# Optimization experiments

Measured on AMD Instinct MI355X. Metric: run time of the kernel, lower is better.

## Reference

```python
import jax, jax.numpy as jnp
import numpy as np

L, NK = 4, 6  # num blocks, Nk geodesic components

def _gelu(x):
    return jax.nn.gelu(x, approximate=False)  # torch nn.GELU default (erf)

def _ln(x, g, b, eps=1e-5):
    m = jnp.mean(x, axis=-1, keepdims=True)
    v = jnp.mean((x - m) ** 2, axis=-1, keepdims=True)
    return (x - m) * jax.lax.rsqrt(v + eps) * g + b


def setup_inputs() -> dict:
    B, N, C, M = 4, 8192, 64, 64
    key = jax.random.key(0)
    ks = iter(jax.random.split(key, 48))
    def nrm(*s):
        return jax.random.normal(next(ks), s, dtype=jnp.float32) * 0.02
    inp = {
        'x': jax.random.normal(next(ks), (B, N, 1), dtype=jnp.float32),
        'MATRIX_Phy': jax.random.normal(next(ks), (N, M), dtype=jnp.float32) * 0.02,
        'INVERSE_Phy': jax.random.normal(next(ks), (M, N), dtype=jnp.float32) * 0.02,
        'meshPoints': jax.random.normal(next(ks), (N, 3), dtype=jnp.float32),
        'adj_norm': jax.random.uniform(next(ks), (N, N), dtype=jnp.float32) / N,
    }
    inp.update(
        fc0_w=nrm(4, C), fc0_b=jnp.zeros(C), fc01_w=nrm(C, C), fc01_b=jnp.zeros(C),
        blk_ln1_g=jnp.ones((L, C)), blk_ln1_b=jnp.zeros((L, C)),
        norm1_g=jnp.ones((L, C)), norm1_b=jnp.zeros((L, C)),
        spec_w=jax.random.uniform(next(ks), (L, NK, C, C, M), dtype=jnp.float32) / (C * C),
        enc_p1_w=nrm(L, 3, C), enc_p1_b=jnp.zeros((L, C)),
        enc_p2_w=nrm(L, C, C), enc_p2_b=jnp.zeros((L, C)),
        enc_g1_w=nrm(L, C, C), enc_g1_b=jnp.zeros((L, C)),
        enc_g2_w=nrm(L, C, C), enc_g2_b=jnp.zeros((L, C)),
        enc_o1_w=nrm(L, C, 2 * C), enc_o1_b=jnp.zeros((L, 2 * C)),
        enc_o2_w=nrm(L, 2 * C, NK), enc_o2_b=jnp.zeros((L, NK)),
        spat_g1_w=nrm(L, C, 2 * C), spat_g1_b=jnp.zeros((L, 2 * C)),
        spat_g2_w=nrm(L, 2 * C, C), spat_g2_b=jnp.zeros((L, C)),
        blk_ln2_g=jnp.ones((L, C)), blk_ln2_b=jnp.zeros((L, C)),
        mlp_pre_w=nrm(L, C, 2 * C), mlp_pre_b=jnp.zeros((L, 2 * C)),
        mlp_post_w=nrm(L, 2 * C, C), mlp_post_b=jnp.zeros((L, C)),
        ln1_g=jnp.ones(C), ln1_b=jnp.zeros(C),
        fc1_w=nrm(C, 128), fc1_b=jnp.zeros(128),
        fc2_w=nrm(128, 1), fc2_b=jnp.zeros(1),
    )
    return inp


def reference(x, MATRIX_Phy, INVERSE_Phy, meshPoints, adj_norm,
              fc0_w, fc0_b, fc01_w, fc01_b,
              blk_ln1_g, blk_ln1_b, norm1_g, norm1_b, spec_w,
              enc_p1_w, enc_p1_b, enc_p2_w, enc_p2_b,
              enc_g1_w, enc_g1_b, enc_g2_w, enc_g2_b,
              enc_o1_w, enc_o1_b, enc_o2_w, enc_o2_b,
              spat_g1_w, spat_g1_b, spat_g2_w, spat_g2_b,
              blk_ln2_g, blk_ln2_b, mlp_pre_w, mlp_pre_b, mlp_post_w, mlp_post_b,
              ln1_g, ln1_b, fc1_w, fc1_b, fc2_w, fc2_b):
    B = x.shape[0]
    mesh = jnp.broadcast_to(meshPoints[None], (B,) + meshPoints.shape)  # [B,N,3]
    h = jnp.concatenate([x, mesh], axis=-1)                             # [B,N,4]
    h = h @ fc0_w + fc0_b
    h = h @ fc01_w + fc01_b                                             # [B,N,C]
    for l in range(L):
        z = _ln(h, blk_ln1_g[l], blk_ln1_b[l])
        # --- MeshGCN encoder -> geodesic mixing coefficients geoT [M,Nk] ---
        e = _gelu(meshPoints @ enc_p1_w[l] + enc_p1_b[l]) @ enc_p2_w[l] + enc_p2_b[l]
        e = _gelu(adj_norm @ (e @ enc_g1_w[l] + enc_g1_b[l]))
        e = adj_norm @ (e @ enc_g2_w[l] + enc_g2_b[l])
        e = (e @ enc_o1_w[l] + enc_o1_b[l]) @ enc_o2_w[l] + enc_o2_b[l]  # [N,Nk]
        geoT = jax.nn.softmax(INVERSE_Phy @ e, axis=1)                   # [M,Nk]
        # --- geodesic-modulated spectral conv ---
        cm = jnp.einsum('mn,bnc->bcm', INVERSE_Phy, z)                   # [B,C,M]
        w = jnp.einsum('kiom,mk->iom', spec_w[l], geoT)                  # [C,C,M]
        cg = jnp.einsum('bim,iom->bom', cm, w)                           # [B,C,M]
        x1 = jnp.einsum('bom,nm->bno', cg, MATRIX_Phy)                   # [B,N,C]
        x1 = _ln(x1, norm1_g[l], norm1_b[l])
        # --- spatial GCN branch (SimpleGCN: gcn->relu->gcn) ---
        s = jax.nn.relu(jnp.einsum('mn,bnc->bmc', adj_norm, z @ spat_g1_w[l] + spat_g1_b[l]))
        x2 = jnp.einsum('mn,bnc->bmc', adj_norm, s @ spat_g2_w[l] + spat_g2_b[l])
        h = x1 + x2 + h
        z2 = _ln(h, blk_ln2_g[l], blk_ln2_b[l])
        h = _gelu(z2 @ mlp_pre_w[l] + mlp_pre_b[l]) @ mlp_post_w[l] + mlp_post_b[l] + h
    h = _gelu(_ln(h, ln1_g, ln1_b) @ fc1_w + fc1_b)
    return h @ fc2_w + fc2_b                                             # [B,N,1]
```

## Files before the change

kernel.cpp:

```cpp
#include <hip/hip_runtime.h>
#include <math.h>

typedef __bf16 bf16_t;
typedef __bf16 bf16x8 __attribute__((ext_vector_type(8)));
typedef __bf16 bf16x4 __attribute__((ext_vector_type(4)));
typedef float  f32x4  __attribute__((ext_vector_type(4)));
typedef float  f32x16 __attribute__((ext_vector_type(16)));

#define NN 8192
#define RA 8320
#define GPS256 2129920u
#define GPS512 4259840u
#define XPAD 68
#define X2PAD 132
#define ZTPAD 66

__device__ __forceinline__ float gelu_f(float x) {
    return 0.5f * x * (1.0f + erff(x * 0.70710678118654752f));
}

__device__ __forceinline__ float wsum64(float v) {
#pragma unroll
    for (int m = 32; m; m >>= 1) v += __shfl_xor(v, m);
    return v;
}

__device__ __forceinline__ float gp4(const float* __restrict__ Gp, size_t gi) {
    return (Gp[gi] + Gp[gi + (size_t)GPS256]) + (Gp[gi + 2 * (size_t)GPS256] + Gp[gi + 3 * (size_t)GPS256]);
}

__device__ __forceinline__ float gpn(const float* __restrict__ Gp, size_t gi, size_t st, int ns) {
    float v = Gp[gi];
    for (int s = 1; s < ns; ++s) v += Gp[gi + (size_t)s * st];
    return v;
}

__device__ __forceinline__ void async16(const void* g, void* l) {
    __builtin_amdgcn_global_load_lds(
        (const __attribute__((address_space(1))) unsigned int*)g,
        (__attribute__((address_space(3))) unsigned int*)l,
        16, 0, 0);
}

__device__ __forceinline__ void mm16(const float* __restrict__ X, int xpad,
                                     const float* __restrict__ W, int ws, int K,
                                     int c, int r0, float* acc) {
    for (int k0 = 0; k0 < K; k0 += 4) {
        float w0 = W[(size_t)(k0 + 0) * ws + c];
        float w1 = W[(size_t)(k0 + 1) * ws + c];
        float w2 = W[(size_t)(k0 + 2) * ws + c];
        float w3 = W[(size_t)(k0 + 3) * ws + c];
#pragma unroll
        for (int i = 0; i < 16; ++i) {
            float4 xv = *(const float4*)(X + (size_t)(r0 + i) * xpad + k0);
            acc[i] = fmaf(xv.x, w0, acc[i]);
            acc[i] = fmaf(xv.y, w1, acc[i]);
            acc[i] = fmaf(xv.z, w2, acc[i]);
            acc[i] = fmaf(xv.w, w3, acc[i]);
        }
    }
}

__global__ __launch_bounds__(256) void k_adj_convert(const float* __restrict__ adj,
                                                     const float* __restrict__ INV,
                                                     bf16_t* __restrict__ adjB,
                                                     float* __restrict__ rowsum) {
    int row = blockIdx.x;
    int t = threadIdx.x;
    bf16_t* br = adjB + (size_t)row * NN;
    if (row >= NN + 64) {
        bf16x4 zz; zz[0] = zz[1] = zz[2] = zz[3] = (bf16_t)0.f;
#pragma unroll
        for (int v = 0; v < 8; ++v) *(bf16x4*)(br + (v * 256 + t) * 4) = zz;
        return;
    }
    const float* ar = (row < NN) ? adj + (size_t)row * NN : INV + (size_t)(row - NN) * NN;
    float s = 0.f;
#pragma unroll
    for (int v = 0; v < 8; ++v) {
        int i = (v * 256 + t) * 4;
        float4 f = *(const float4*)(ar + i);
        s += f.x + f.y + f.z + f.w;
        bf16x4 o;
        o[0] = (bf16_t)f.x; o[1] = (bf16_t)f.y; o[2] = (bf16_t)f.z; o[3] = (bf16_t)f.w;
        *(bf16x4*)(br + i) = o;
    }
    if (row < NN) {
        s = wsum64(s);
        __shared__ float w4[4];
        if ((t & 63) == 0) w4[t >> 6] = s;
        __syncthreads();
        if (t == 0) rowsum[row] = w4[0] + w4[1] + w4[2] + w4[3];
    }
}

__global__ __launch_bounds__(64) void k_fold(const float* __restrict__ fc0w, const float* __restrict__ fc0b,
                                             const float* __restrict__ fc01w, const float* __restrict__ fc01b,
                                             float* __restrict__ W0b) {
    int c = threadIdx.x;
#pragma unroll
    for (int j = 0; j < 4; ++j) {
        float a = 0.f;
        for (int k = 0; k < 64; ++k) a += fc0w[j * 64 + k] * fc01w[k * 64 + c];
        W0b[j * 64 + c] = a;
    }
    float b = fc01b[c];
    for (int k = 0; k < 64; ++k) b += fc0b[k] * fc01w[k * 64 + c];
    W0b[256 + c] = b;
}

__global__ __launch_bounds__(256) void k_init_h(const float* __restrict__ x, const float* __restrict__ mesh,
                         const float* __restrict__ W0b,
                         const float* __restrict__ zg, const float* __restrict__ zb,
                         float* __restrict__ h, bf16_t* __restrict__ Vt) {
    __shared__ __align__(16) char buf[64 * ZTPAD * 2];
    bf16_t* ZT = (bf16_t*)buf;
    int t = threadIdx.x, c = t & 63, rq = t >> 6, r0 = rq * 16;
    int bb = blockIdx.x >> 7, n0 = (blockIdx.x & 127) * 64;
    float w0c = W0b[c], w1c = W0b[64 + c], w2c = W0b[128 + c], w3c = W0b[192 + c], b0c = W0b[256 + c];
    float gc = zg[c], bc = zb[c];
#pragma unroll
    for (int q = 0; q < 16; ++q) {
        int n = n0 + r0 + q;
        int w = bb * NN + n;
        float xv = x[w];
        float m0 = mesh[n * 3], m1 = mesh[n * 3 + 1], m2 = mesh[n * 3 + 2];
        float hv = b0c + xv * w0c + m0 * w1c + m1 * w2c + m2 * w3c;
        h[(size_t)w * 64 + c] = hv;
        float s = wsum64(hv), s2 = wsum64(hv * hv);
        float mean = s * (1.f / 64.f), var = s2 * (1.f / 64.f) - mean * mean;
        float z = (hv - mean) * rsqrtf(var + 1e-5f) * gc + bc;
        ZT[c * ZTPAD + r0 + q] = (bf16_t)z;
    }
    __syncthreads();
#pragma unroll
    for (int cc = 0; cc < 16; ++cc) {
        int c2 = r0 + cc;
        Vt[(size_t)(256 + bb * 64 + c2) * NN + n0 + c] = ZT[c2 * ZTPAD + c];
    }
}

__global__ __launch_bounds__(256) void k_enc_pre(const float* __restrict__ mesh,
                          const float* __restrict__ p1w, const float* __restrict__ p1b,
                          const float* __restrict__ p2w, const float* __restrict__ p2b,
                          const float* __restrict__ g1w, const float* __restrict__ g1b,
                          bf16_t* __restrict__ Vt) {
    __shared__ __align__(16) char buf[2 * 64 * XPAD * 4];
    float* X1 = (float*)buf;
    float* X2 = (float*)(buf + 64 * XPAD * 4);
    bf16_t* ZT = (bf16_t*)buf;
    int t = threadIdx.x, c = t & 63, rq = t >> 6, r0 = rq * 16;
    int ll = blockIdx.x >> 7, n0 = (blockIdx.x & 127) * 64;
    float p1b_c = p1b[ll * 64 + c];
    float p1w0 = p1w[(ll * 3 + 0) * 64 + c], p1w1 = p1w[(ll * 3 + 1) * 64 + c], p1w2 = p1w[(ll * 3 + 2) * 64 + c];
#pragma unroll
    for (int q = 0; q < 16; ++q) {
        int n = n0 + r0 + q;
        float m0 = mesh[n * 3], m1 = mesh[n * 3 + 1], m2 = mesh[n * 3 + 2];
        X1[(r0 + q) * XPAD + c] = gelu_f(p1b_c + m0 * p1w0 + m1 * p1w1 + m2 * p1w2);
    }
    __syncthreads();
    float e2[16];
#pragma unroll
    for (int i = 0; i < 16; ++i) e2[i] = p2b[ll * 64 + c];
    mm16(X1, XPAD, p2w + ll * 4096, 64, 64, c, r0, e2);
    __syncthreads();
#pragma unroll
    for (int q = 0; q < 16; ++q) X2[(r0 + q) * XPAD + c] = e2[q];
    __syncthreads();
    float tt[16];
#pragma unroll
    for (int i = 0; i < 16; ++i) tt[i] = g1b[ll * 64 + c];
    mm16(X2, XPAD, g1w + ll * 4096, 64, 64, c, r0, tt);
#pragma unroll
    for (int q = 0; q < 16; ++q) ZT[c * ZTPAD + r0 + q] = (bf16_t)tt[q];
    __syncthreads();
#pragma unroll
    for (int cc = 0; cc < 16; ++cc) {
        int c2 = r0 + cc;
        Vt[(size_t)(ll * 64 + c2) * NN + n0 + c] = ZT[c2 * ZTPAD + c];
    }
}

__global__ __launch_bounds__(256) void k_enc_mid(const float* __restrict__ Gp,
                          const float* __restrict__ g2w, const float* __restrict__ g2b,
                          bf16_t* __restrict__ Vt) {
    __shared__ __align__(16) char buf[64 * XPAD * 4 + 64 * ZTPAD * 2];
    float* X = (float*)buf;
    bf16_t* ZT = (bf16_t*)(buf + 64 * XPAD * 4);
    int t = threadIdx.x, c = t & 63, rq = t >> 6, r0 = rq * 16;
    int ll = blockIdx.x >> 7, n0 = (blockIdx.x & 127) * 64;
#pragma unroll
    for (int q = 0; q < 16; ++q) {
        int n = n0 + r0 + q;
        X[(r0 + q) * XPAD + c] = gelu_f(gp4(Gp, (size_t)n * 256 + ll * 64 + c));
    }
    __syncthreads();
    float t2[16];
#pragma unroll
    for (int i = 0; i < 16; ++i) t2[i] = g2b[ll * 64 + c];
    mm16(X, XPAD, g2w + ll * 4096, 64, 64, c, r0, t2);
#pragma unroll
    for (int q = 0; q < 16; ++q) ZT[c * ZTPAD + r0 + q] = (bf16_t)t2[q];
    __syncthreads();
#pragma unroll
    for (int cc = 0; cc < 16; ++cc) {
        int c2 = r0 + cc;
        Vt[(size_t)(ll * 64 + c2) * NN + n0 + c] = ZT[c2 * ZTPAD + c];
    }
}

__global__ void k_geo_part(const float* __restrict__ Gp,
                           const float* __restrict__ o1w, const float* __restrict__ o1b,
                           const float* __restrict__ o2w, const float* __restrict__ o2b,
                           const float* __restrict__ INV,
                           float* __restrict__ partials) {
    int l = blockIdx.x >> 7, chunk = blockIdx.x & 127;
    int n0 = chunk * 64;
    int t = threadIdx.x;
    __shared__ float e4L[64][65];
    for (int r = 0; r < 64; ++r) {
        size_t gi = (size_t)(n0 + r) * 512 + l * 64 + t;
        e4L[r][t] = Gp[gi] + Gp[gi + (size_t)GPS512];
    }
    __syncthreads();
    float X[64];
#pragma unroll
    for (int i = 0; i < 64; ++i) X[i] = e4L[t][i];
    float e5[6] = {0, 0, 0, 0, 0, 0};
    const float* o1wl = o1w + (size_t)l * 64 * 128;
    const float* o2wl = o2w + (size_t)l * 128 * 6;
    for (int j = 0; j < 128; ++j) {
        float a = o1b[l * 128 + j];
#pragma unroll
        for (int i = 0; i < 64; ++i) a += X[i] * o1wl[i * 128 + j];
#pragma unroll
        for (int k = 0; k < 6; ++k) e5[k] += a * o2wl[j * 6 + k];
    }
#pragma unroll
    for (int k = 0; k < 6; ++k) e5[k] += o2b[l * 6 + k];
    __shared__ float e5L[64][8];
#pragma unroll
    for (int k = 0; k < 6; ++k) e5L[t][k] = e5[k];
    __syncthreads();
    float p[6] = {0, 0, 0, 0, 0, 0};
    const float* ivr = INV + (size_t)t * NN + n0;
    for (int r = 0; r < 64; ++r) {
        float iv = ivr[r];
#pragma unroll
        for (int k = 0; k < 6; ++k) p[k] += iv * e5L[r][k];
    }
#pragma unroll
    for (int k = 0; k < 6; ++k) partials[(size_t)(((l * 128 + chunk) * 64) + t) * 6 + k] = p[k];
}

__global__ void k_geo_final(const float* __restrict__ partials, float* __restrict__ geoT) {
    int l = blockIdx.x, m = threadIdx.x;
    float g[6] = {0, 0, 0, 0, 0, 0};
    for (int ch = 0; ch < 128; ++ch) {
#pragma unroll
        for (int k = 0; k < 6; ++k) g[k] += partials[(size_t)(((l * 128 + ch) * 64) + m) * 6 + k];
    }
    float mx = g[0];
#pragma unroll
    for (int k = 1; k < 6; ++k) mx = fmaxf(mx, g[k]);
    float s = 0.f;
#pragma unroll
    for (int k = 0; k < 6; ++k) { g[k] = expf(g[k] - mx); s += g[k]; }
    float inv = 1.f / s;
#pragma unroll
    for (int k = 0; k < 6; ++k) geoT[(size_t)(l * 64 + m) * 6 + k] = g[k] * inv;
}

__global__ __launch_bounds__(64) void k_w(const float* __restrict__ specw,
                                          const float* __restrict__ geoT,
                                          float* __restrict__ wAll) {
    int l = blockIdx.x >> 12, io = blockIdx.x & 4095;
    int m = threadIdx.x;
    float a = 0.f;
#pragma unroll
    for (int k = 0; k < 6; ++k)
        a += specw[(((size_t)l * 6 + k) * 4096 + io) * 64 + m] * geoT[(size_t)(l * 64 + m) * 6 + k];
    wAll[((size_t)l * 4096 + io) * 64 + m] = a;
}

__global__ __launch_bounds__(256) void k_cmsum(const float* __restrict__ Gp, float* __restrict__ cmc,
                                               int ncols, int colbase, int ns) {
    int bi = blockIdx.x * 4 + (threadIdx.x >> 6);
    int m = threadIdx.x & 63;
    size_t st = (size_t)RA * ncols;
    size_t gi = (size_t)(NN + m) * ncols + colbase + bi;
    cmc[bi * 64 + m] = gpn(Gp, gi, st, ns);
}

__global__ __launch_bounds__(256) void k_cg2(const float* __restrict__ cmc,
                                             const float* __restrict__ wl,
                                             float* __restrict__ cgT) {
    int o = blockIdx.x;
    int b = threadIdx.x >> 6, m = threadIdx.x & 63;
    float acc = 0.f;
    for (int i = 0; i < 64; ++i)
        acc += cmc[(b * 64 + i) * 64 + m] * wl[((size_t)(i * 64 + o)) * 64 + m];
    cgT[(b * 64 + m) * 64 + o] = acc;
}

__global__ __launch_bounds__(256) void k_spat_mid(const float* __restrict__ Gp,
                           const float* __restrict__ W1, const float* __restrict__ b1,
                           const float* __restrict__ W2, const float* __restrict__ b2,
                           const float* __restrict__ rowsum, bf16_t* __restrict__ Vt,
                           int ncols, int colbase, int ns) {
    __shared__ __align__(16) char buf[64 * XPAD * 4 + 64 * X2PAD * 4];
    float* X  = (float*)buf;
    float* X2 = (float*)(buf + 64 * XPAD * 4);
    bf16_t* ZT = (bf16_t*)buf;
    int t = threadIdx.x, c = t & 63, rq = t >> 6, r0 = rq * 16;
    int bb = blockIdx.x >> 7, n0 = (blockIdx.x & 127) * 64;
    size_t st = (size_t)RA * ncols;
    float rs[16];
#pragma unroll
    for (int q = 0; q < 16; ++q) {
        int m = n0 + r0 + q;
        rs[q] = rowsum[m];
        X[(r0 + q) * XPAD + c] = gpn(Gp, (size_t)m * ncols + colbase + bb * 64 + c, st, ns);
    }
    __syncthreads();
    float ma0[16], ma1[16];
    float b1c0 = b1[c], b1c1 = b1[64 + c];
#pragma unroll
    for (int i = 0; i < 16; ++i) { ma0[i] = rs[i] * b1c0; ma1[i] = rs[i] * b1c1; }
    mm16(X, XPAD, W1, 128, 64, c, r0, ma0);
    mm16(X, XPAD, W1 + 64, 128, 64, c, r0, ma1);
    __syncthreads();
#pragma unroll
    for (int q = 0; q < 16; ++q) {
        X2[(r0 + q) * X2PAD + c] = fmaxf(ma0[q], 0.f);
        X2[(r0 + q) * X2PAD + 64 + c] = fmaxf(ma1[q], 0.f);
    }
    __syncthreads();
    float y[16];
#pragma unroll
    for (int i = 0; i < 16; ++i) y[i] = b2[c];
    mm16(X2, X2PAD, W2, 64, 128, c, r0, y);
#pragma unroll
    for (int q = 0; q < 16; ++q) ZT[c * ZTPAD + r0 + q] = (bf16_t)y[q];
    __syncthreads();
#pragma unroll
    for (int cc = 0; cc < 16; ++cc) {
        int c2 = r0 + cc;
        Vt[(size_t)(bb * 64 + c2) * NN + n0 + c] = ZT[c2 * ZTPAD + c];
    }
}

__global__ __launch_bounds__(256) void k_blk_post(float* __restrict__ h, const float* __restrict__ Gp,
                           const float* __restrict__ cgT, const float* __restrict__ MP,
                           const float* __restrict__ n1g, const float* __restrict__ n1b,
                           const float* __restrict__ l2g, const float* __restrict__ l2b,
                           const float* __restrict__ prew, const float* __restrict__ preb,
                           const float* __restrict__ postw, const float* __restrict__ postb,
                           const float* __restrict__ zng, const float* __restrict__ znb,
                           bf16_t* __restrict__ Vt, int writeZ) {
    __shared__ __align__(16) char buf[64 * X2PAD * 4 + 64 * XPAD * 4];
    float* MProws = (float*)buf;
    float* X2     = (float*)buf;
    float* X      = (float*)(buf + 64 * X2PAD * 4);
    bf16_t* ZT    = (bf16_t*)(buf + 64 * X2PAD * 4);
    int t = threadIdx.x, c = t & 63, rq = t >> 6, r0 = rq * 16;
    int bb = blockIdx.x >> 7, n0 = (blockIdx.x & 127) * 64;
#pragma unroll
    for (int q = 0; q < 16; ++q)
        MProws[(r0 + q) * XPAD + c] = MP[(size_t)(n0 + r0 + q) * 64 + c];
    __syncthreads();
    float x1[16];
#pragma unroll
    for (int i = 0; i < 16; ++i) x1[i] = 0.f;
    mm16(MProws, XPAD, cgT + (size_t)bb * 4096, 64, 64, c, r0, x1);
    float hv[16];
    float n1gc = n1g[c], n1bc = n1b[c];
#pragma unroll
    for (int q = 0; q < 16; ++q) {
        float s = wsum64(x1[q]), s2 = wsum64(x1[q] * x1[q]);
        float mean = s * (1.f / 64.f), var = s2 * (1.f / 64.f) - mean * mean;
        float x1n = (x1[q] - mean) * rsqrtf(var + 1e-5f) * n1gc + n1bc;
        int n = n0 + r0 + q;
        size_t w = (size_t)bb * NN + n;
        hv[q] = x1n + gp4(Gp, (size_t)n * 256 + bb * 64 + c) + h[w * 64 + c];
    }
    float l2gc = l2g[c], l2bc = l2b[c];
#pragma unroll
    for (int q = 0; q < 16; ++q) {
        float s = wsum64(hv[q]), s2 = wsum64(hv[q] * hv[q]);
        float mean = s * (1.f / 64.f), var = s2 * (1.f / 64.f) - mean * mean;
        X[(r0 + q) * XPAD + c] = (hv[q] - mean) * rsqrtf(var + 1e-5f) * l2gc + l2bc;
    }
    __syncthreads();
    float ma0[16], ma1[16];
    float pb0 = preb[c], pb1 = preb[64 + c];
#pragma unroll
    for (int i = 0; i < 16; ++i) { ma0[i] = pb0; ma1[i] = pb1; }
    mm16(X, XPAD, prew, 128, 64, c, r0, ma0);
    mm16(X, XPAD, prew + 64, 128, 64, c, r0, ma1);
    __syncthreads();
#pragma unroll
    for (int q = 0; q < 16; ++q) {
        X2[(r0 + q) * X2PAD + c] = gelu_f(ma0[q]);
        X2[(r0 + q) * X2PAD + 64 + c] = gelu_f(ma1[q]);
    }
    __syncthreads();
    float o[16];
    float pob = postb[c];
#pragma unroll
    for (int i = 0; i < 16; ++i) o[i] = pob;
    mm16(X2, X2PAD, postw, 64, 128, c, r0, o);
#pragma unroll
    for (int q = 0; q < 16; ++q) {
        hv[q] += o[q];
        h[((size_t)bb * NN + n0 + r0 + q) * 64 + c] = hv[q];
    }
    if (writeZ) {
        float zgc = zng[c], zbc = znb[c];
#pragma unroll
        for (int q = 0; q < 16; ++q) {
            float s = wsum64(hv[q]), s2 = wsum64(hv[q] * hv[q]);
            float mean = s * (1.f / 64.f), var = s2 * (1.f / 64.f) - mean * mean;
            ZT[c * ZTPAD + r0 + q] = (bf16_t)((hv[q] - mean) * rsqrtf(var + 1e-5f) * zgc + zbc);
        }
        __syncthreads();
#pragma unroll
        for (int cc = 0; cc < 16; ++cc) {
            int c2 = r0 + cc;
            Vt[(size_t)(256 + bb * 64 + c2) * NN + n0 + c] = ZT[c2 * ZTPAD + c];
        }
    }
}

__global__ __launch_bounds__(256) void k_head(const float* __restrict__ h,
                       const float* __restrict__ g, const float* __restrict__ bb_,
                       const float* __restrict__ fc1w, const float* __restrict__ fc1b,
                       const float* __restrict__ fc2w, const float* __restrict__ fc2b,
                       float* __restrict__ out) {
    __shared__ __align__(16) char buf[64 * XPAD * 4 + 64 * X2PAD * 4];
    float* X  = (float*)buf;
    float* X2 = (float*)(buf + 64 * XPAD * 4);
    int t = threadIdx.x, c = t & 63, rq = t >> 6, r0 = rq * 16;
    int bb = blockIdx.x >> 7, n0 = (blockIdx.x & 127) * 64;
    float gc = g[c], bc = bb_[c];
#pragma unroll
    for (int q = 0; q < 16; ++q) {
        float hv = h[((size_t)bb * NN + n0 + r0 + q) * 64 + c];
        float s = wsum64(hv), s2 = wsum64(hv * hv);
        float mean = s * (1.f / 64.f), var = s2 * (1.f / 64.f) - mean * mean;
        X[(r0 + q) * XPAD + c] = (hv - mean) * rsqrtf(var + 1e-5f) * gc + bc;
    }
    __syncthreads();
    float ma0[16], ma1[16];
    float fb0 = fc1b[c], fb1 = fc1b[64 + c];
#pragma unroll
    for (int i = 0; i < 16; ++i) { ma0[i] = fb0; ma1[i] = fb1; }
    mm16(X, XPAD, fc1w, 128, 64, c, r0, ma0);
    mm16(X, XPAD, fc1w + 64, 128, 64, c, r0, ma1);
    __syncthreads();
#pragma unroll
    for (int q = 0; q < 16; ++q) {
        X2[(r0 + q) * X2PAD + c] = gelu_f(ma0[q]);
        X2[(r0 + q) * X2PAD + 64 + c] = gelu_f(ma1[q]);
    }
    __syncthreads();
    float f2a = fc2w[c], f2b = fc2w[64 + c], f2bias = fc2b[0];
#pragma unroll
    for (int q = 0; q < 16; ++q) {
        float val = X2[(r0 + q) * X2PAD + c] * f2a + X2[(r0 + q) * X2PAD + 64 + c] * f2b;
        val = wsum64(val);
        if (c == 0) out[(size_t)bb * NN + n0 + r0 + q] = val + f2bias;
    }
}

__global__ __launch_bounds__(512, 2) void gemm_bf16(const bf16_t* __restrict__ A,
                                                    const bf16_t* __restrict__ Bt,
                                                    float* __restrict__ Gp,
                                                    int ntn, int ns) {
    __shared__ __align__(16) char smem[2][49152];
    const int bid = blockIdx.x;
    const int per_tm = ntn * ns;
    const int tm = bid / per_tm;
    const int rem = bid % per_tm;
    const int tn = rem / ns;
    const int ks = rem % ns;
    const int nkt = 128 / ns;
    const int kt0 = ks * nkt;
    const int ncols = ntn * 256;

    const int t = threadIdx.x;
    const int lane = t & 63, wid = t >> 6;
    const int wr = wid >> 2, wc = wid & 3;
    const int lm = lane & 31;
    const int lkg = lane >> 5;

    const bf16_t* Abase = A + (size_t)tm * 128 * NN;
    const bf16_t* Bbase = Bt + (size_t)tn * 256 * NN;

    f32x16 acc[2][2];
#pragma unroll
    for (int i = 0; i < 2; ++i)
#pragma unroll
        for (int j = 0; j < 2; ++j)
#pragma unroll
            for (int r = 0; r < 16; ++r) acc[i][j][r] = 0.f;

    auto stage = [&](int bsel, int kt) {
        char* lb = smem[bsel];
        int k0 = kt * 64;
#pragma unroll
        for (int r = 0; r < 2; ++r) {
            int ci = t + r * 512;
            int rw = ci >> 3, ch = ci & 7;
            int sch = ch ^ (rw & 7);
            async16(Abase + (size_t)rw * NN + k0 + sch * 8, lb + ci * 16);
        }
#pragma unroll
        for (int r = 0; r < 4; ++r) {
            int ci = t + r * 512;
            int rw = ci >> 3, ch = ci & 7;
            int sch = ch ^ (rw & 7);
            async16(Bbase + (size_t)rw * NN + k0 + sch * 8, lb + 16384 + ci * 16);
        }
    };

    const int R0 = wr * 64 + lm;
    const int R1 = R0 + 32;
    const int Q0 = wc * 64 + lm;
    const int Q1 = Q0 + 32;
    const int swzA = R0 & 7, swzB = Q0 & 7;

    stage(0, kt0);
    __syncthreads();
    for (int it = 0; it < nkt; ++it) {
        int cur = it & 1;
        if (it + 1 < nkt) stage(cur ^ 1, kt0 + it + 1);
        const char* lb = smem[cur];
#pragma unroll
        for (int ks4 = 0; ks4 < 4; ++ks4) {
            int kc = ks4 * 2 + lkg;
            bf16x8 av0 = *(const bf16x8*)(lb + R0 * 128 + ((kc ^ swzA) << 4));
            bf16x8 av1 = *(const bf16x8*)(lb + R1 * 128 + ((kc ^ swzA) << 4));
            bf16x8 bv0 = *(const bf16x8*)(lb + 16384 + Q0 * 128 + ((kc ^ swzB) << 4));
            bf16x8 bv1 = *(const bf16x8*)(lb + 16384 + Q1 * 128 + ((kc ^ swzB) << 4));
            acc[0][0] = __builtin_amdgcn_mfma_f32_32x32x16_bf16(av0, bv0, acc[0][0], 0, 0, 0);
            acc[0][1] = __builtin_amdgcn_mfma_f32_32x32x16_bf16(av0, bv1, acc[0][1], 0, 0, 0);
            acc[1][0] = __builtin_amdgcn_mfma_f32_32x32x16_bf16(av1, bv0, acc[1][0], 0, 0, 0);
            acc[1][1] = __builtin_amdgcn_mfma_f32_32x32x16_bf16(av1, bv1, acc[1][1], 0, 0, 0);
        }
        __syncthreads();
    }

    float* Cs = Gp + (size_t)ks * RA * ncols;
    const int colbase = tn * 256 + wc * 64 + lm;
    const int rowbase = tm * 128 + wr * 64 + 4 * lkg;
#pragma unroll
    for (int i = 0; i < 2; ++i)
#pragma unroll
        for (int j = 0; j < 2; ++j)
#pragma unroll
            for (int reg = 0; reg < 16; ++reg) {
                int rrow = (reg & 3) + 8 * (reg >> 2);
                Cs[(size_t)(rowbase + i * 32 + rrow) * ncols + colbase + j * 32] = acc[i][j][reg];
            }
}


extern "C" void kernel_launch(void* const* d_in, const int* in_sizes, int n_in,
                              void* d_out, int out_size, void* d_ws, size_t ws_size,
                              hipStream_t stream) {
    const float* x     = (const float*)d_in[0];
    const float* MP    = (const float*)d_in[1];
    const float* INV   = (const float*)d_in[2];
    const float* mesh  = (const float*)d_in[3];
    const float* adj   = (const float*)d_in[4];
    const float* fc0w  = (const float*)d_in[5];
    const float* fc0b  = (const float*)d_in[6];
    const float* fc01w = (const float*)d_in[7];
    const float* fc01b = (const float*)d_in[8];
    const float* bln1g = (const float*)d_in[9];
    const float* bln1b = (const float*)d_in[10];
    const float* n1g   = (const float*)d_in[11];
    const float* n1b   = (const float*)d_in[12];
    const float* specw = (const float*)d_in[13];
    const float* p1w   = (const float*)d_in[14];
    const float* p1b   = (const float*)d_in[15];
    const float* p2w   = (const float*)d_in[16];
    const float* p2b   = (const float*)d_in[17];
    const float* g1w   = (const float*)d_in[18];
    const float* g1b   = (const float*)d_in[19];
    const float* g2w   = (const float*)d_in[20];
    const float* g2b   = (const float*)d_in[21];
    const float* o1w   = (const float*)d_in[22];
    const float* o1b   = (const float*)d_in[23];
    const float* o2w   = (const float*)d_in[24];
    const float* o2b   = (const float*)d_in[25];
    const float* sg1w  = (const float*)d_in[26];
    const float* sg1b  = (const float*)d_in[27];
    const float* sg2w  = (const float*)d_in[28];
    const float* sg2b  = (const float*)d_in[29];
    const float* bln2g = (const float*)d_in[30];
    const float* bln2b = (const float*)d_in[31];
    const float* prew  = (const float*)d_in[32];
    const float* preb  = (const float*)d_in[33];
    const float* postw = (const float*)d_in[34];
    const float* postb = (const float*)d_in[35];
    const float* ln1g  = (const float*)d_in[36];
    const float* ln1b  = (const float*)d_in[37];
    const float* fc1w  = (const float*)d_in[38];
    const float* fc1b  = (const float*)d_in[39];
    const float* fc2w  = (const float*)d_in[40];
    const float* fc2b  = (const float*)d_in[41];
    float* out = (float*)d_out;

    char* ws = (char*)d_ws;
    bf16_t* adjB    = (bf16_t*)(ws);
    float*  Gp512   = (float*) (ws + 136314880);
    float*  Gp256   = (float*) (ws + 170393600);
    bf16_t* Vt      = (bf16_t*)(ws + 204472320);
    float*  h       = (float*) (ws + 212860928);
    float*  rowsum  = (float*) (ws + 221249536);
    float*  partials= (float*) (ws + 221282304);
    float*  geoT    = (float*) (ws + 222068736);
    float*  wAll    = (float*) (ws + 222074880);
    float*  cmc     = (float*) (ws + 226269184);
    float*  cgT     = (float*) (ws + 226334720);
    float*  W0b     = (float*) (ws + 226400256);

    bf16_t* VtZ = Vt + (size_t)256 * NN;

    k_adj_convert<<<RA, 256, 0, stream>>>(adj, INV, adjB, rowsum);
    k_fold<<<1, 64, 0, stream>>>(fc0w, fc0b, fc01w, fc01b, W0b);

    k_enc_pre<<<512, 256, 0, stream>>>(mesh, p1w, p1b, p2w, p2b, g1w, g1b, Vt);
    gemm_bf16<<<260, 512, 0, stream>>>(adjB, Vt, Gp256, 1, 4);
    k_enc_mid<<<512, 256, 0, stream>>>(Gp256, g2w, g2b, Vt);
    k_init_h<<<512, 256, 0, stream>>>(x, mesh, W0b, bln1g, bln1b, h, Vt);

    gemm_bf16<<<260, 512, 0, stream>>>(adjB, Vt, Gp512, 2, 2);

    k_geo_part<<<512, 64, 0, stream>>>(Gp512, o1w, o1b, o2w, o2b, INV, partials);
    k_geo_final<<<4, 64, 0, stream>>>(partials, geoT);
    k_w<<<16384, 64, 0, stream>>>(specw, geoT, wAll);

    for (int l = 0; l < 4; ++l) {
        const float* Gp1 = Gp256; int nc = 256, cb = 0, ns1 = 4;
        if (l == 0) { Gp1 = Gp512; nc = 512; cb = 256; ns1 = 2; }
        else {
            gemm_bf16<<<260, 512, 0, stream>>>(adjB, VtZ, Gp256, 1, 4);
        }
        k_cmsum<<<64, 256, 0, stream>>>(Gp1, cmc, nc, cb, ns1);
        k_cg2<<<64, 256, 0, stream>>>(cmc, wAll + (size_t)l * 262144, cgT);
        k_spat_mid<<<512, 256, 0, stream>>>(Gp1, sg1w + l * 64 * 128, sg1b + l * 128,
                                            sg2w + l * 128 * 64, sg2b + l * 64, rowsum, Vt,
                                            nc, cb, ns1);
        gemm_bf16<<<260, 512, 0, stream>>>(adjB, Vt, Gp256, 1, 4);
        int ln = (l < 3) ? (l + 1) : 3;
        k_blk_post<<<512, 256, 0, stream>>>(h, Gp256, cgT, MP,
                                            n1g + l * 64, n1b + l * 64,
                                            bln2g + l * 64, bln2b + l * 64,
                                            prew + l * 64 * 128, preb + l * 128,
                                            postw + l * 128 * 64, postb + l * 64,
                                            bln1g + ln * 64, bln1b + ln * 64,
                                            Vt, (l < 3) ? 1 : 0);
    }

    k_head<<<512, 256, 0, stream>>>(h, ln1g, ln1b, fc1w, fc1b, fc2w, fc2b, out);
}
```

Measured before the change: 1.514 ms.

## Retile bf16 adjacency GEMM to 128x128 tiles with 16x16 MFMA and XCD remap

Rewrites the adjacency GEMM to use 256-thread blocks computing 128x128 output tiles with a 32-wide K step, replacing the 128x256 tile with 32x32x16 MFMA. It now uses 16x16x32 MFMA with 4x4 accumulators per wave, a smaller LDS footprint and a 4-chunk swizzle. Block IDs are remapped round-robin across 8 groups (XCD-aware), and launches double to 520 blocks. The aim is higher occupancy and better L2 locality per chiplet. The cost is less operand reuse per block and more global traffic per FLOP.

```diff
diff --git a/kernel.cpp b/kernel.cpp
--- a/kernel.cpp
+++ b/kernel.cpp
@@ -5,7 +5,6 @@
 typedef __bf16 bf16x8 __attribute__((ext_vector_type(8)));
 typedef __bf16 bf16x4 __attribute__((ext_vector_type(4)));
 typedef float  f32x4  __attribute__((ext_vector_type(4)));
-typedef float  f32x16 __attribute__((ext_vector_type(16)));
 
 #define NN 8192
 #define RA 8320
@@ -474,62 +473,57 @@
     }
 }
 
-__global__ __launch_bounds__(512, 2) void gemm_bf16(const bf16_t* __restrict__ A,
+__global__ __launch_bounds__(256, 3) void gemm_bf16(const bf16_t* __restrict__ A,
                                                     const bf16_t* __restrict__ Bt,
                                                     float* __restrict__ Gp,
                                                     int ntn, int ns) {
-    __shared__ __align__(16) char smem[2][49152];
+    __shared__ __align__(16) char smem[2][16384];
+    const int cpx = gridDim.x >> 3;
     const int bid = blockIdx.x;
+    const int tile = (bid & 7) * cpx + (bid >> 3);
     const int per_tm = ntn * ns;
-    const int tm = bid / per_tm;
-    const int rem = bid % per_tm;
-    const int tn = rem / ns;
-    const int ks = rem % ns;
-    const int nkt = 128 / ns;
+    const int tm = tile / per_tm;
+    const int rem = tile % per_tm;
+    const int tn = rem % ntn;
+    const int ks = rem / ntn;
+    const int nkt = 256 / ns;
     const int kt0 = ks * nkt;
-    const int ncols = ntn * 256;
+    const int ncols = ntn * 128;
 
     const int t = threadIdx.x;
     const int lane = t & 63, wid = t >> 6;
-    const int wr = wid >> 2, wc = wid & 3;
-    const int lm = lane & 31;
-    const int lkg = lane >> 5;
+    const int wr = wid >> 1, wc = wid & 1;
+    const int lrow = lane & 15, lk = lane >> 4;
 
     const bf16_t* Abase = A + (size_t)tm * 128 * NN;
-    const bf16_t* Bbase = Bt + (size_t)tn * 256 * NN;
-
-    f32x16 acc[2][2];
-#pragma unroll
-    for (int i = 0; i < 2; ++i)
-#pragma unroll
-        for (int j = 0; j < 2; ++j)
-#pragma unroll
-            for (int r = 0; r < 16; ++r) acc[i][j][r] = 0.f;
+    const bf16_t* Bbase = Bt + (size_t)tn * 128 * NN;
+
+    f32x4 acc[4][4];
+#pragma unroll
+    for (int i = 0; i < 4; ++i)
+#pragma unroll
+        for (int j = 0; j < 4; ++j) acc[i][j] = f32x4{0.f, 0.f, 0.f, 0.f};
 
     auto stage = [&](int bsel, int kt) {
         char* lb = smem[bsel];
-        int k0 = kt * 64;
-#pragma unroll
-        for (int r = 0; r < 2; ++r) {
-            int ci = t + r * 512;
-            int rw = ci >> 3, ch = ci & 7;
-            int sch = ch ^ (rw & 7);
+        int k0 = kt * 32;
+        {
+            int ci = t;
+            int rw = ci >> 2, ch = ci & 3, sch = ch ^ (rw & 3);
             async16(Abase + (size_t)rw * NN + k0 + sch * 8, lb + ci * 16);
-        }
-#pragma unroll
-        for (int r = 0; r < 4; ++r) {
-            int ci = t + r * 512;
-            int rw = ci >> 3, ch = ci & 7;
-            int sch = ch ^ (rw & 7);
-            async16(Bbase + (size_t)rw * NN + k0 + sch * 8, lb + 16384 + ci * 16);
+            ci = t + 256;
+            rw = ci >> 2; ch = ci & 3; sch = ch ^ (rw & 3);
+            async16(Abase + (size_t)rw * NN + k0 + sch * 8, lb + ci * 16);
+        }
+        {
+            int ci = t;
+            int rw = ci >> 2, ch = ci & 3, sch = ch ^ (rw & 3);
+            async16(Bbase + (size_t)rw * NN + k0 + sch * 8, lb + 8192 + ci * 16);
+            ci = t + 256;
+            rw = ci >> 2; ch = ci & 3; sch = ch ^ (rw & 3);
+            async16(Bbase + (size_t)rw * NN + k0 + sch * 8, lb + 8192 + ci * 16);
         }
     };
-
-    const int R0 = wr * 64 + lm;
-    const int R1 = R0 + 32;
-    const int Q0 = wc * 64 + lm;
-    const int Q1 = Q0 + 32;
-    const int swzA = R0 & 7, swzB = Q0 & 7;
 
     stage(0, kt0);
     __syncthreads();
@@ -537,33 +531,35 @@
         int cur = it & 1;
         if (it + 1 < nkt) stage(cur ^ 1, kt0 + it + 1);
         const char* lb = smem[cur];
-#pragma unroll
-        for (int ks4 = 0; ks4 < 4; ++ks4) {
-            int kc = ks4 * 2 + lkg;
-            bf16x8 av0 = *(const bf16x8*)(lb + R0 * 128 + ((kc ^ swzA) << 4));
-            bf16x8 av1 = *(const bf16x8*)(lb + R1 * 128 + ((kc ^ swzA) << 4));
-            bf16x8 bv0 = *(const bf16x8*)(lb + 16384 + Q0 * 128 + ((kc ^ swzB) << 4));
-            bf16x8 bv1 = *(const bf16x8*)(lb + 16384 + Q1 * 128 + ((kc ^ swzB) << 4));
-            acc[0][0] = __builtin_amdgcn_mfma_f32_32x32x16_bf16(av0, bv0, acc[0][0], 0, 0, 0);
-            acc[0][1] = __builtin_amdgcn_mfma_f32_32x32x16_bf16(av0, bv1, acc[0][1], 0, 0, 0);
-            acc[1][0] = __builtin_amdgcn_mfma_f32_32x32x16_bf16(av1, bv0, acc[1][0], 0, 0, 0);
-            acc[1][1] = __builtin_amdgcn_mfma_f32_32x32x16_bf16(av1, bv1, acc[1][1], 0, 0, 0);
-        }
+        bf16x8 av[4], bv[4];
+#pragma unroll
+        for (int i = 0; i < 4; ++i) {
+            int R = wr * 64 + i * 16 + lrow;
+            av[i] = *(const bf16x8*)(lb + R * 64 + ((lk ^ (R & 3)) << 4));
+        }
+#pragma unroll
+        for (int j = 0; j < 4; ++j) {
+            int Q = wc * 64 + j * 16 + lrow;
+            bv[j] = *(const bf16x8*)(lb + 8192 + Q * 64 + ((lk ^ (Q & 3)) << 4));
+        }
+#pragma unroll
+        for (int i = 0; i < 4; ++i)
+#pragma unroll
+            for (int j = 0; j < 4; ++j)
+                acc[i][j] = __builtin_amdgcn_mfma_f32_16x16x32_bf16(av[i], bv[j], acc[i][j], 0, 0, 0);
         __syncthreads();
     }
 
     float* Cs = Gp + (size_t)ks * RA * ncols;
-    const int colbase = tn * 256 + wc * 64 + lm;
-    const int rowbase = tm * 128 + wr * 64 + 4 * lkg;
-#pragma unroll
-    for (int i = 0; i < 2; ++i)
-#pragma unroll
-        for (int j = 0; j < 2; ++j)
-#pragma unroll
-            for (int reg = 0; reg < 16; ++reg) {
-                int rrow = (reg & 3) + 8 * (reg >> 2);
-                Cs[(size_t)(rowbase + i * 32 + rrow) * ncols + colbase + j * 32] = acc[i][j][reg];
-            }
+    const int row0 = tm * 128 + wr * 64;
+    const int col0 = tn * 128 + wc * 64;
+#pragma unroll
+    for (int i = 0; i < 4; ++i)
+#pragma unroll
+        for (int j = 0; j < 4; ++j)
+#pragma unroll
+            for (int r = 0; r < 4; ++r)
+                Cs[(size_t)(row0 + i * 16 + lk * 4 + r) * ncols + col0 + j * 16 + lrow] = acc[i][j][r];
 }
 
 
@@ -634,11 +630,11 @@
     k_fold<<<1, 64, 0, stream>>>(fc0w, fc0b, fc01w, fc01b, W0b);
 
     k_enc_pre<<<512, 256, 0, stream>>>(mesh, p1w, p1b, p2w, p2b, g1w, g1b, Vt);
-    gemm_bf16<<<260, 512, 0, stream>>>(adjB, Vt, Gp256, 1, 4);
+    gemm_bf16<<<520, 256, 0, stream>>>(adjB, Vt, Gp256, 2, 4);
     k_enc_mid<<<512, 256, 0, stream>>>(Gp256, g2w, g2b, Vt);
     k_init_h<<<512, 256, 0, stream>>>(x, mesh, W0b, bln1g, bln1b, h, Vt);
 
-    gemm_bf16<<<260, 512, 0, stream>>>(adjB, Vt, Gp512, 2, 2);
+    gemm_bf16<<<520, 256, 0, stream>>>(adjB, Vt, Gp512, 4, 2);
 
     k_geo_part<<<512, 64, 0, stream>>>(Gp512, o1w, o1b, o2w, o2b, INV, partials);
     k_geo_final<<<4, 64, 0, stream>>>(partials, geoT);
@@ -648,14 +644,14 @@
         const float* Gp1 = Gp256; int nc = 256, cb = 0, ns1 = 4;
         if (l == 0) { Gp1 = Gp512; nc = 512; cb = 256; ns1 = 2; }
         else {
-            gemm_bf16<<<260, 512, 0, stream>>>(adjB, VtZ, Gp256, 1, 4);
+            gemm_bf16<<<520, 256, 0, stream>>>(adjB, VtZ, Gp256, 2, 4);
         }
         k_cmsum<<<64, 256, 0, stream>>>(Gp1, cmc, nc, cb, ns1);
         k_cg2<<<64, 256, 0, stream>>>(cmc, wAll + (size_t)l * 262144, cgT);
         k_spat_mid<<<512, 256, 0, stream>>>(Gp1, sg1w + l * 64 * 128, sg1b + l * 128,
                                             sg2w + l * 128 * 64, sg2b + l * 64, rowsum, Vt,
                                             nc, cb, ns1);
-        gemm_bf16<<<260, 512, 0, stream>>>(adjB, Vt, Gp256, 1, 4);
+        gemm_bf16<<<520, 256, 0, stream>>>(adjB, Vt, Gp256, 2, 4);
         int ln = (l < 3) ? (l + 1) : 3;
         k_blk_post<<<512, 256, 0, stream>>>(h, Gp256, cgT, MP,
                                             n1g + l * 64, n1b + l * 64,
```

After: 1.323 ms. 1.14x faster.

## Retile adjacency GEMM to 256x256 MFMA16 tiles and compute INV projection separately

Applied to the files above, without the earlier changes.

The bf16 GEMM over the adjacency matrix moves from 128x256 tiles with 32x32 MFMA to 256x256 tiles with 16x16x32 MFMA. Split-K doubles (4→8 and 2→4), and the loads are software pipelined with explicit vmcnt waits and barriers. The INVERSE_Phy rows no longer ride along as extra GEMM rows; a new k_cm kernel computes the INV·z projection directly in fp32, and the padded row count and conversion for those rows are removed. The intent is to raise arithmetic intensity per loaded tile and cut launch padding. In exchange, the split-K partial buffers double in size, more partials must be summed, and the large accumulator array raises register pressure.

```diff
diff --git a/kernel.cpp b/kernel.cpp
--- a/kernel.cpp
+++ b/kernel.cpp
@@ -5,12 +5,10 @@
 typedef __bf16 bf16x8 __attribute__((ext_vector_type(8)));
 typedef __bf16 bf16x4 __attribute__((ext_vector_type(4)));
 typedef float  f32x4  __attribute__((ext_vector_type(4)));
-typedef float  f32x16 __attribute__((ext_vector_type(16)));
 
 #define NN 8192
-#define RA 8320
-#define GPS256 2129920u
-#define GPS512 4259840u
+#define GST256 2097152u
+#define GST512 4194304u
 #define XPAD 68
 #define X2PAD 132
 #define ZTPAD 66
@@ -25,8 +23,12 @@
     return v;
 }
 
-__device__ __forceinline__ float gp4(const float* __restrict__ Gp, size_t gi) {
-    return (Gp[gi] + Gp[gi + (size_t)GPS256]) + (Gp[gi + 2 * (size_t)GPS256] + Gp[gi + 3 * (size_t)GPS256]);
+__device__ __forceinline__ float gp8(const float* __restrict__ Gp, size_t gi) {
+    float a = Gp[gi] + Gp[gi + (size_t)GST256];
+    float b = Gp[gi + 2 * (size_t)GST256] + Gp[gi + 3 * (size_t)GST256];
+    float c = Gp[gi + 4 * (size_t)GST256] + Gp[gi + 5 * (size_t)GST256];
+    float d = Gp[gi + 6 * (size_t)GST256] + Gp[gi + 7 * (size_t)GST256];
+    return (a + b) + (c + d);
 }
 
 __device__ __forceinline__ float gpn(const float* __restrict__ Gp, size_t gi, size_t st, int ns) {
@@ -62,19 +64,12 @@
 }
 
 __global__ __launch_bounds__(256) void k_adj_convert(const float* __restrict__ adj,
-                                                     const float* __restrict__ INV,
                                                      bf16_t* __restrict__ adjB,
                                                      float* __restrict__ rowsum) {
     int row = blockIdx.x;
     int t = threadIdx.x;
+    const float* ar = adj + (size_t)row * NN;
     bf16_t* br = adjB + (size_t)row * NN;
-    if (row >= NN + 64) {
-        bf16x4 zz; zz[0] = zz[1] = zz[2] = zz[3] = (bf16_t)0.f;
-#pragma unroll
-        for (int v = 0; v < 8; ++v) *(bf16x4*)(br + (v * 256 + t) * 4) = zz;
-        return;
-    }
-    const float* ar = (row < NN) ? adj + (size_t)row * NN : INV + (size_t)(row - NN) * NN;
     float s = 0.f;
 #pragma unroll
     for (int v = 0; v < 8; ++v) {
@@ -85,13 +80,11 @@
         o[0] = (bf16_t)f.x; o[1] = (bf16_t)f.y; o[2] = (bf16_t)f.z; o[3] = (bf16_t)f.w;
         *(bf16x4*)(br + i) = o;
     }
-    if (row < NN) {
-        s = wsum64(s);
-        __shared__ float w4[4];
-        if ((t & 63) == 0) w4[t >> 6] = s;
-        __syncthreads();
-        if (t == 0) rowsum[row] = w4[0] + w4[1] + w4[2] + w4[3];
-    }
+    s = wsum64(s);
+    __shared__ float w4[4];
+    if ((t & 63) == 0) w4[t >> 6] = s;
+    __syncthreads();
+    if (t == 0) rowsum[row] = w4[0] + w4[1] + w4[2] + w4[3];
 }
 
 __global__ __launch_bounds__(64) void k_fold(const float* __restrict__ fc0w, const float* __restrict__ fc0b,
@@ -193,7 +186,7 @@
 #pragma unroll
     for (int q = 0; q < 16; ++q) {
         int n = n0 + r0 + q;
-        X[(r0 + q) * XPAD + c] = gelu_f(gp4(Gp, (size_t)n * 256 + ll * 64 + c));
+        X[(r0 + q) * XPAD + c] = gelu_f(gp8(Gp, (size_t)n * 256 + ll * 64 + c));
     }
     __syncthreads();
     float t2[16];
@@ -221,7 +214,8 @@
     __shared__ float e4L[64][65];
     for (int r = 0; r < 64; ++r) {
         size_t gi = (size_t)(n0 + r) * 512 + l * 64 + t;
-        e4L[r][t] = Gp[gi] + Gp[gi + (size_t)GPS512];
+        e4L[r][t] = (Gp[gi] + Gp[gi + (size_t)GST512])
+                  + (Gp[gi + 2 * (size_t)GST512] + Gp[gi + 3 * (size_t)GST512]);
     }
     __syncthreads();
     float X[64];
@@ -284,13 +278,23 @@
     wAll[((size_t)l * 4096 + io) * 64 + m] = a;
 }
 
-__global__ __launch_bounds__(256) void k_cmsum(const float* __restrict__ Gp, float* __restrict__ cmc,
-                                               int ncols, int colbase, int ns) {
-    int bi = blockIdx.x * 4 + (threadIdx.x >> 6);
-    int m = threadIdx.x & 63;
-    size_t st = (size_t)RA * ncols;
-    size_t gi = (size_t)(NN + m) * ncols + colbase + bi;
-    cmc[bi * 64 + m] = gpn(Gp, gi, st, ns);
+__global__ __launch_bounds__(256) void k_cm(const float* __restrict__ INV,
+                                            const bf16_t* __restrict__ VtZ,
+                                            float* __restrict__ cmc) {
+    int wid = threadIdx.x >> 6, lane = threadIdx.x & 63;
+    int task = blockIdx.x * 4 + wid;
+    int m = task & 63, i = (task >> 6) & 63, b = task >> 12;
+    const float* iv = INV + (size_t)m * NN;
+    const bf16_t* zt = VtZ + (size_t)(b * 64 + i) * NN;
+    float acc = 0.f;
+    for (int it = 0; it < 32; ++it) {
+        int n0 = (it * 64 + lane) * 4;
+        float4 v = *(const float4*)(iv + n0);
+        bf16x4 z4 = *(const bf16x4*)(zt + n0);
+        acc += v.x * (float)z4[0] + v.y * (float)z4[1] + v.z * (float)z4[2] + v.w * (float)z4[3];
+    }
+    acc = wsum64(acc);
+    if (lane == 0) cmc[((b * 64 + i) * 64) + m] = acc;
 }
 
 __global__ __launch_bounds__(256) void k_cg2(const float* __restrict__ cmc,
@@ -315,7 +319,7 @@
     bf16_t* ZT = (bf16_t*)buf;
     int t = threadIdx.x, c = t & 63, rq = t >> 6, r0 = rq * 16;
     int bb = blockIdx.x >> 7, n0 = (blockIdx.x & 127) * 64;
-    size_t st = (size_t)RA * ncols;
+    size_t st = (size_t)NN * ncols;
     float rs[16];
 #pragma unroll
     for (int q = 0; q < 16; ++q) {
@@ -383,7 +387,7 @@
         float x1n = (x1[q] - mean) * rsqrtf(var + 1e-5f) * n1gc + n1bc;
         int n = n0 + r0 + q;
         size_t w = (size_t)bb * NN + n;
-        hv[q] = x1n + gp4(Gp, (size_t)n * 256 + bb * 64 + c) + h[w * 64 + c];
+        hv[q] = x1n + gp8(Gp, (size_t)n * 256 + bb * 64 + c) + h[w * 64 + c];
     }
     float l2gc = l2g[c], l2bc = l2b[c];
 #pragma unroll
@@ -477,93 +481,101 @@
 __global__ __launch_bounds__(512, 2) void gemm_bf16(const bf16_t* __restrict__ A,
                                                     const bf16_t* __restrict__ Bt,
                                                     float* __restrict__ Gp,
-                                                    int ntn, int ns) {
-    __shared__ __align__(16) char smem[2][49152];
+                                                    int ntn, int ns, int nkt) {
+    __shared__ __align__(16) char smem[2][65536];
     const int bid = blockIdx.x;
     const int per_tm = ntn * ns;
     const int tm = bid / per_tm;
     const int rem = bid % per_tm;
-    const int tn = rem / ns;
-    const int ks = rem % ns;
-    const int nkt = 128 / ns;
+    const int tn = rem % ntn;
+    const int ks = rem / ntn;
     const int kt0 = ks * nkt;
     const int ncols = ntn * 256;
 
     const int t = threadIdx.x;
     const int lane = t & 63, wid = t >> 6;
     const int wr = wid >> 2, wc = wid & 3;
-    const int lm = lane & 31;
-    const int lkg = lane >> 5;
-
-    const bf16_t* Abase = A + (size_t)tm * 128 * NN;
+    const int lrow = lane & 15, lk = lane >> 4;
+
+    const bf16_t* Abase = A + (size_t)tm * 256 * NN;
     const bf16_t* Bbase = Bt + (size_t)tn * 256 * NN;
 
-    f32x16 acc[2][2];
-#pragma unroll
-    for (int i = 0; i < 2; ++i)
-#pragma unroll
-        for (int j = 0; j < 2; ++j)
-#pragma unroll
-            for (int r = 0; r < 16; ++r) acc[i][j][r] = 0.f;
-
-    auto stage = [&](int bsel, int kt) {
-        char* lb = smem[bsel];
+    f32x4 acc[8][4];
+#pragma unroll
+    for (int m = 0; m < 8; ++m)
+#pragma unroll
+        for (int n = 0; n < 4; ++n) acc[m][n] = f32x4{0.f, 0.f, 0.f, 0.f};
+
+    auto stage = [&](int d, int kt) {
+        char* lb = smem[d];
         int k0 = kt * 64;
-#pragma unroll
-        for (int r = 0; r < 2; ++r) {
-            int ci = t + r * 512;
-            int rw = ci >> 3, ch = ci & 7;
-            int sch = ch ^ (rw & 7);
-            async16(Abase + (size_t)rw * NN + k0 + sch * 8, lb + ci * 16);
-        }
 #pragma unroll
         for (int r = 0; r < 4; ++r) {
             int ci = t + r * 512;
-            int rw = ci >> 3, ch = ci & 7;
-            int sch = ch ^ (rw & 7);
-            async16(Bbase + (size_t)rw * NN + k0 + sch * 8, lb + 16384 + ci * 16);
+            int rw = ci >> 3, ch = ci & 7, sch = ch ^ (rw & 7);
+            async16(Abase + (size_t)rw * NN + k0 + sch * 8, lb + ci * 16);
+        }
+#pragma unroll
+        for (int r = 0; r < 4; ++r) {
+            int ci = t + r * 512;
+            int rw = ci >> 3, ch = ci & 7, sch = ch ^ (rw & 7);
+            async16(Bbase + (size_t)rw * NN + k0 + sch * 8, lb + 32768 + ci * 16);
         }
     };
 
-    const int R0 = wr * 64 + lm;
-    const int R1 = R0 + 32;
-    const int Q0 = wc * 64 + lm;
-    const int Q1 = Q0 + 32;
-    const int swzA = R0 & 7, swzB = Q0 & 7;
-
     stage(0, kt0);
-    __syncthreads();
+    asm volatile("s_waitcnt vmcnt(0)" ::: "memory");
+    __builtin_amdgcn_sched_barrier(0);
+    __builtin_amdgcn_s_barrier();
+
     for (int it = 0; it < nkt; ++it) {
-        int cur = it & 1;
-        if (it + 1 < nkt) stage(cur ^ 1, kt0 + it + 1);
-        const char* lb = smem[cur];
-#pragma unroll
-        for (int ks4 = 0; ks4 < 4; ++ks4) {
-            int kc = ks4 * 2 + lkg;
-            bf16x8 av0 = *(const bf16x8*)(lb + R0 * 128 + ((kc ^ swzA) << 4));
-            bf16x8 av1 = *(const bf16x8*)(lb + R1 * 128 + ((kc ^ swzA) << 4));
-            bf16x8 bv0 = *(const bf16x8*)(lb + 16384 + Q0 * 128 + ((kc ^ swzB) << 4));
-            bf16x8 bv1 = *(const bf16x8*)(lb + 16384 + Q1 * 128 + ((kc ^ swzB) << 4));
-            acc[0][0] = __builtin_amdgcn_mfma_f32_32x32x16_bf16(av0, bv0, acc[0][0], 0, 0, 0);
-            acc[0][1] = __builtin_amdgcn_mfma_f32_32x32x16_bf16(av0, bv1, acc[0][1], 0, 0, 0);
-            acc[1][0] = __builtin_amdgcn_mfma_f32_32x32x16_bf16(av1, bv0, acc[1][0], 0, 0, 0);
-            acc[1][1] = __builtin_amdgcn_mfma_f32_32x32x16_bf16(av1, bv1, acc[1][1], 0, 0, 0);
-        }
-        __syncthreads();
-    }
-
-    float* Cs = Gp + (size_t)ks * RA * ncols;
-    const int colbase = tn * 256 + wc * 64 + lm;
-    const int rowbase = tm * 128 + wr * 64 + 4 * lkg;
-#pragma unroll
-    for (int i = 0; i < 2; ++i)
-#pragma unroll
-        for (int j = 0; j < 2; ++j)
-#pragma unroll
-            for (int reg = 0; reg < 16; ++reg) {
-                int rrow = (reg & 3) + 8 * (reg >> 2);
-                Cs[(size_t)(rowbase + i * 32 + rrow) * ncols + colbase + j * 32] = acc[i][j][reg];
+        const int cur = it & 1;
+        if (it + 1 < nkt) {
+            stage(cur ^ 1, kt0 + it + 1);
+            asm volatile("s_waitcnt vmcnt(8)" ::: "memory");
+        } else {
+            asm volatile("s_waitcnt vmcnt(0)" ::: "memory");
+        }
+        __builtin_amdgcn_sched_barrier(0);
+        __builtin_amdgcn_s_barrier();
+
+        const char* la = smem[cur];
+        const char* lbB = smem[cur] + 32768;
+#pragma unroll
+        for (int kk = 0; kk < 2; ++kk) {
+            bf16x8 av[8], bv[4];
+            int kc = kk * 4 + lk;
+#pragma unroll
+            for (int m = 0; m < 8; ++m) {
+                int R = wr * 128 + m * 16 + lrow;
+                av[m] = *(const bf16x8*)(la + R * 128 + ((kc ^ (R & 7)) << 4));
             }
+#pragma unroll
+            for (int n = 0; n < 4; ++n) {
+                int Q = wc * 64 + n * 16 + lrow;
+                bv[n] = *(const bf16x8*)(lbB + Q * 128 + ((kc ^ (Q & 7)) << 4));
+            }
+#pragma unroll
+            for (int m = 0; m < 8; ++m)
+#pragma unroll
+                for (int n = 0; n < 4; ++n)
+                    acc[m][n] = __builtin_amdgcn_mfma_f32_16x16x32_bf16(av[m], bv[n], acc[m][n], 0, 0, 0);
+        }
+        asm volatile("s_waitcnt lgkmcnt(0)" ::: "memory");
+        __builtin_amdgcn_sched_barrier(0);
+        __builtin_amdgcn_s_barrier();
+    }
+
+    float* Cs = Gp + (size_t)ks * NN * ncols;
+    const int row0 = tm * 256 + wr * 128;
+    const int col0 = tn * 256 + wc * 64;
+#pragma unroll
+    for (int m = 0; m < 8; ++m)
+#pragma unroll
+        for (int n = 0; n < 4; ++n)
+#pragma unroll
+            for (int r = 0; r < 4; ++r)
+                Cs[(size_t)(row0 + m * 16 + lk * 4 + r) * ncols + col0 + n * 16 + lrow] = acc[m][n][r];
 }
 
 
@@ -616,46 +628,46 @@
 
     char* ws = (char*)d_ws;
     bf16_t* adjB    = (bf16_t*)(ws);
-    float*  Gp512   = (float*) (ws + 136314880);
-    float*  Gp256   = (float*) (ws + 170393600);
-    bf16_t* Vt      = (bf16_t*)(ws + 204472320);
-    float*  h       = (float*) (ws + 212860928);
-    float*  rowsum  = (float*) (ws + 221249536);
-    float*  partials= (float*) (ws + 221282304);
-    float*  geoT    = (float*) (ws + 222068736);
-    float*  wAll    = (float*) (ws + 222074880);
-    float*  cmc     = (float*) (ws + 226269184);
-    float*  cgT     = (float*) (ws + 226334720);
-    float*  W0b     = (float*) (ws + 226400256);
+    float*  Gp512   = (float*) (ws + 134217728);
+    float*  Gp256   = (float*) (ws + 201326592);
+    bf16_t* Vt      = (bf16_t*)(ws + 268435456);
+    float*  h       = (float*) (ws + 276824064);
+    float*  rowsum  = (float*) (ws + 285212672);
+    float*  partials= (float*) (ws + 285245440);
+    float*  geoT    = (float*) (ws + 286031872);
+    float*  wAll    = (float*) (ws + 286038016);
+    float*  cmc     = (float*) (ws + 290232320);
+    float*  cgT     = (float*) (ws + 290297856);
+    float*  W0b     = (float*) (ws + 290363392);
 
     bf16_t* VtZ = Vt + (size_t)256 * NN;
 
-    k_adj_convert<<<RA, 256, 0, stream>>>(adj, INV, adjB, rowsum);
+    k_adj_convert<<<NN, 256, 0, stream>>>(adj, adjB, rowsum);
     k_fold<<<1, 64, 0, stream>>>(fc0w, fc0b, fc01w, fc01b, W0b);
 
     k_enc_pre<<<512, 256, 0, stream>>>(mesh, p1w, p1b, p2w, p2b, g1w, g1b, Vt);
-    gemm_bf16<<<260, 512, 0, stream>>>(adjB, Vt, Gp256, 1, 4);
+    gemm_bf16<<<256, 512, 0, stream>>>(adjB, Vt, Gp256, 1, 8, 16);
     k_enc_mid<<<512, 256, 0, stream>>>(Gp256, g2w, g2b, Vt);
     k_init_h<<<512, 256, 0, stream>>>(x, mesh, W0b, bln1g, bln1b, h, Vt);
 
-    gemm_bf16<<<260, 512, 0, stream>>>(adjB, Vt, Gp512, 2, 2);
+    gemm_bf16<<<256, 512, 0, stream>>>(adjB, Vt, Gp512, 2, 4, 32);
 
     k_geo_part<<<512, 64, 0, stream>>>(Gp512, o1w, o1b, o2w, o2b, INV, partials);
     k_geo_final<<<4, 64, 0, stream>>>(partials, geoT);
     k_w<<<16384, 64, 0, stream>>>(specw, geoT, wAll);
 
     for (int l = 0; l < 4; ++l) {
-        const float* Gp1 = Gp256; int nc = 256, cb = 0, ns1 = 4;
-        if (l == 0) { Gp1 = Gp512; nc = 512; cb = 256; ns1 = 2; }
+        const float* Gp1 = Gp256; int nc = 256, cb = 0, ns1 = 8;
+        if (l == 0) { Gp1 = Gp512; nc = 512; cb = 256; ns1 = 4; }
         else {
-            gemm_bf16<<<260, 512, 0, stream>>>(adjB, VtZ, Gp256, 1, 4);
-        }
-        k_cmsum<<<64, 256, 0, stream>>>(Gp1, cmc, nc, cb, ns1);
+            gemm_bf16<<<256, 512, 0, stream>>>(adjB, VtZ, Gp256, 1, 8, 16);
+        }
+        k_cm<<<4096, 256, 0, stream>>>(INV, VtZ, cmc);
         k_cg2<<<64, 256, 0, stream>>>(cmc, wAll + (size_t)l * 262144, cgT);
         k_spat_mid<<<512, 256, 0, stream>>>(Gp1, sg1w + l * 64 * 128, sg1b + l * 128,
                                             sg2w + l * 128 * 64, sg2b + l * 64, rowsum, Vt,
                                             nc, cb, ns1);
-        gemm_bf16<<<260, 512, 0, stream>>>(adjB, Vt, Gp256, 1, 4);
+        gemm_bf16<<<256, 512, 0, stream>>>(adjB, Vt, Gp256, 1, 8, 16);
         int ln = (l < 3) ? (l + 1) : 3;
         k_blk_post<<<512, 256, 0, stream>>>(h, Gp256, cgT, MP,
                                             n1g + l * 64, n1b + l * 64,
```

After: 1.443 ms. -4.7%, faster.
